# Kernel tuning notes

Hardware: AMD Instinct MI355X
Metric: run time of the kernel (lower is better)

Reference implementation:

```python
import jax, jax.numpy as jnp
import numpy as np

B, N, C = 4, 262144, 10
K_PRE, K_POST = 4096, 500          # before_nms_max, after_nms_max
ROI_THR, NMS_THR = 0.1, 0.01       # roi_threshold, nms_threshold


def setup_inputs() -> dict:
    key = jax.random.key(0)
    k1, k2, k3, k4 = jax.random.split(key, 4)
    # raw logits; sigmoid(-2 + noise) straddles roi_threshold=0.1 realistically
    cls = jax.random.normal(k1, (B, N, C), jnp.float32) - 2.0
    centers = jax.random.uniform(k2, (B, N, 3), jnp.float32, minval=-50.0, maxval=50.0)
    sizes = jax.random.uniform(k3, (B, N, 3), jnp.float32, minval=0.5, maxval=5.0)
    heading = jax.random.uniform(k4, (B, N, 1), jnp.float32, minval=-np.pi, maxval=np.pi)
    boxes = jnp.concatenate([centers, sizes, heading], axis=-1)  # (B, N, 7)
    return {"batch_cls_preds": cls, "batch_box_preds": boxes}


def _pairwise_bev_iou(b):
    # b: (K, 7) = [x, y, z, dx, dy, dz, heading]; BEV IoU (heading ignored,
    # axis-aligned approximation of the rotated-IoU CUDA kernel).
    x, y, dx, dy = b[:, 0], b[:, 1], b[:, 3], b[:, 4]
    x1, x2 = x - dx * 0.5, x + dx * 0.5
    y1, y2 = y - dy * 0.5, y + dy * 0.5
    ix = jnp.clip(jnp.minimum(x2[:, None], x2[None, :]) - jnp.maximum(x1[:, None], x1[None, :]), 0.0)
    iy = jnp.clip(jnp.minimum(y2[:, None], y2[None, :]) - jnp.maximum(y1[:, None], y1[None, :]), 0.0)
    inter = ix * iy                              # (K, K)
    area = dx * dy                               # (K,)
    union = area[:, None] + area[None, :] - inter
    return inter / jnp.maximum(union, 1e-6)


def _nms_one(scores, labels, boxes):
    # scores: (N,), labels: (N,) int32, boxes: (N, 7)
    s = jnp.where(scores > ROI_THR, scores, -1.0)       # score-threshold filter
    topv, topi = jax.lax.top_k(s, K_PRE)                # keep top before_nms_max
    tb = boxes[topi]                                     # (K_PRE, 7)
    tl = labels[topi]
    iou = _pairwise_bev_iou(tb)                          # (K_PRE, K_PRE)
    keep0 = topv > ROI_THR

    def body(i, keep):
        # a kept higher-score box i suppresses later boxes with IoU > thr
        sup = (iou[i] > NMS_THR) & (jnp.arange(K_PRE) > i) & keep[i]
        return keep & ~sup

    keep = jax.lax.fori_loop(0, K_PRE, body, keep0)
    kept_scores = jnp.where(keep, topv, -1.0)
    fv, fi = jax.lax.top_k(kept_scores, K_POST)          # after_nms_max slots
    m = fv > 0.0
    final_scores = jnp.where(m, fv, 0.0)                 # (K_POST,)
    final_boxes = tb[fi] * m[:, None].astype(tb.dtype)   # (K_POST, 7)
    final_labels = jnp.where(m, tl[fi], -1)              # (K_POST,)
    return final_scores, final_boxes, final_labels


def reference(batch_cls_preds, batch_box_preds):
    probs = jax.nn.sigmoid(batch_cls_preds)              # (B, N, C)
    scores = jnp.max(probs, axis=-1)                     # per-anchor best class score
    labels = jnp.argmax(probs, axis=-1).astype(jnp.int32)
    final_scores, final_boxes, final_labels = jax.vmap(_nms_one)(scores, labels, batch_box_preds)
    return final_scores, final_boxes, final_labels
```

## Files before the change

kernel.cpp:

```cpp
#include <hip/hip_runtime.h>
#include <stdint.h>

constexpr int B = 4;
constexpr int N = 262144;
constexpr int C = 10;
constexpr int KPRE = 4096;
constexpr int KPOST = 500;
constexpr float ROI_THR = 0.1f;
constexpr float NMS_THR = 0.01f;
constexpr int CAP = 8192;
constexpr int MASKW = KPRE / 64;
constexpr int RJT = 2;
constexpr int MAXP = 32;

__device__ __forceinline__ uint32_t f2k(float f) {
  uint32_t u = __float_as_uint(f);
  return (u & 0x80000000u) ? ~u : (u | 0x80000000u);
}
__device__ __forceinline__ float k2f(uint32_t k) {
  uint32_t u = (k & 0x80000000u) ? (k ^ 0x80000000u) : ~k;
  return __uint_as_float(u);
}
__device__ __forceinline__ float sigm(float x) { return 1.0f / (1.0f + expf(-x)); }

__device__ __forceinline__ void async_lds16(const void* g, void* l) {
  __builtin_amdgcn_global_load_lds((const __attribute__((address_space(1))) void*)g,
                                   (__attribute__((address_space(3))) void*)l, 16, 0, 0);
}

__device__ __forceinline__ uint2 select256(const uint32_t* __restrict__ h, uint32_t R,
                                           uint32_t* s, uint32_t* o2) {
  int t = threadIdx.x;
  s[t] = h[t];
  __syncthreads();
  for (int off = 1; off < 256; off <<= 1) {
    uint32_t v = s[t] + ((t + off < 256) ? s[t + off] : 0u);
    __syncthreads();
    s[t] = v;
    __syncthreads();
  }
  uint32_t suf = s[t];
  uint32_t sufn = (t < 255) ? s[t + 1] : 0u;
  if (suf >= R && R > sufn) {
    o2[0] = (uint32_t)t;
    o2[1] = R - sufn;
  }
  __syncthreads();
  uint2 r;
  r.x = o2[0];
  r.y = o2[1];
  __syncthreads();
  return r;
}

__global__ void scoreK(const float* __restrict__ cls, uint32_t* __restrict__ keys,
                       uint32_t* __restrict__ hist0) {
  __shared__ float ls[2560];
  __shared__ uint32_t h[256];
  int b = blockIdx.y;
  int t = threadIdx.x;
  h[t] = 0;
  size_t base = ((size_t)b * N + (size_t)blockIdx.x * 256) * C;
  const float2* g2 = (const float2*)(cls + base);
  float2* l2 = (float2*)ls;
#pragma unroll
  for (int r = 0; r < 5; ++r) l2[r * 256 + t] = g2[r * 256 + t];
  __syncthreads();
  const float* mine = ls + t * 10;
  float m = mine[0];
#pragma unroll
  for (int c = 1; c < C; ++c) m = fmaxf(m, mine[c]);
  float p = sigm(m);
  float sc = (p > ROI_THR) ? p : -1.0f;
  uint32_t k = f2k(sc);
  keys[(size_t)b * N + blockIdx.x * 256 + t] = k;
  atomicAdd(&h[k >> 24], 1u);
  __syncthreads();
  if (h[t]) atomicAdd(&hist0[b * 256 + t], h[t]);
}

__global__ void histP1K(const uint32_t* __restrict__ keys, const uint32_t* __restrict__ hist0,
                        uint32_t* __restrict__ hist1) {
  __shared__ uint32_t s[256];
  __shared__ uint32_t o2[2];
  __shared__ uint32_t h[256];
  int b = blockIdx.y;
  int t = threadIdx.x;
  uint2 s0 = select256(hist0 + b * 256, (uint32_t)KPRE, s, o2);
  h[t] = 0;
  __syncthreads();
  uint32_t pref = s0.x;
  const uint4* kb4 = (const uint4*)(keys + (size_t)b * N);
#pragma unroll
  for (int r = 0; r < 2; ++r) {
    uint4 kv = kb4[blockIdx.x * 512 + r * 256 + t];
#pragma unroll
    for (int j = 0; j < 4; ++j) {
      uint32_t k = (&kv.x)[j];
      if ((k >> 24) == pref) atomicAdd(&h[(k >> 16) & 255u], 1u);
    }
  }
  __syncthreads();
  if (h[t]) atomicAdd(&hist1[b * 256 + t], h[t]);
}

__global__ void compactK(const uint32_t* __restrict__ keys, const uint32_t* __restrict__ hist0,
                         const uint32_t* __restrict__ hist1, unsigned long long* __restrict__ list,
                         uint32_t* __restrict__ cnt) {
  __shared__ uint32_t s[256];
  __shared__ uint32_t o2[2];
  __shared__ uint32_t scan[256];
  __shared__ uint32_t baseSh;
  int b = blockIdx.y;
  int t = threadIdx.x;
  uint2 s0 = select256(hist0 + b * 256, (uint32_t)KPRE, s, o2);
  uint2 s1 = select256(hist1 + b * 256, s0.y, s, o2);
  uint32_t T = ((s0.x << 8) | s1.x) << 16;
  const uint4* kb4 = (const uint4*)(keys + (size_t)b * N);
  uint4 kv[4];
#pragma unroll
  for (int r = 0; r < 4; ++r) kv[r] = kb4[blockIdx.x * 1024 + r * 256 + t];
  uint32_t c = 0;
#pragma unroll
  for (int r = 0; r < 4; ++r)
#pragma unroll
    for (int j = 0; j < 4; ++j) c += ((&kv[r].x)[j] >= T) ? 1u : 0u;
  scan[t] = c;
  __syncthreads();
  for (int off = 1; off < 256; off <<= 1) {
    uint32_t v = scan[t] + ((t >= off) ? scan[t - off] : 0u);
    __syncthreads();
    scan[t] = v;
    __syncthreads();
  }
  uint32_t excl = scan[t] - c;
  if (t == 255) baseSh = atomicAdd(&cnt[b], scan[255]);
  __syncthreads();
  uint32_t pos = baseSh + excl;
#pragma unroll
  for (int r = 0; r < 4; ++r)
#pragma unroll
    for (int j = 0; j < 4; ++j) {
      uint32_t k = (&kv[r].x)[j];
      if (k >= T) {
        uint32_t n = (blockIdx.x * 1024 + r * 256 + t) * 4 + j;
        if (pos < CAP)
          list[(size_t)b * CAP + pos] = ((unsigned long long)k << 32) | (uint32_t)(~n);
        pos++;
      }
    }
}

__global__ void rankK(const unsigned long long* __restrict__ list, const uint32_t* __restrict__ cnt,
                      uint32_t* __restrict__ rank) {
  __shared__ unsigned long long lp[256];
  int b = blockIdx.z;
  int cc = (int)min(cnt[b], (uint32_t)CAP);
  if (blockIdx.x * 256 >= cc) return;
  int j0 = blockIdx.y * (256 * RJT);
  if (j0 >= cc) return;
  int i = blockIdx.x * 256 + threadIdx.x;
  unsigned long long pi = (i < cc) ? list[(size_t)b * CAP + i] : ~0ull;
  uint32_t c = 0;
#pragma unroll
  for (int tb = 0; tb < RJT; ++tb) {
    int j = j0 + tb * 256 + threadIdx.x;
    __syncthreads();
    lp[threadIdx.x] = (j < cc) ? list[(size_t)b * CAP + j] : 0ull;
    __syncthreads();
#pragma unroll 8
    for (int jj = 0; jj < 256; ++jj) c += (lp[jj] > pi) ? 1u : 0u;
  }
  if (i < cc && c) atomicAdd(&rank[(size_t)b * CAP + i], c);
}

__global__ void scatterK(const unsigned long long* __restrict__ list,
                         const uint32_t* __restrict__ cnt, const uint32_t* __restrict__ rank,
                         const float* __restrict__ boxes, float* __restrict__ sel_score,
                         uint32_t* __restrict__ sel_idx, float* __restrict__ sel_box) {
  int b = blockIdx.y;
  int p = blockIdx.x * 256 + threadIdx.x;
  uint32_t cc = min(cnt[b], (uint32_t)CAP);
  if (p >= (int)cc) return;
  unsigned long long pk = list[(size_t)b * CAP + p];
  uint32_t r = rank[(size_t)b * CAP + p];
  if (r >= (uint32_t)KPRE) return;
  uint32_t key = (uint32_t)(pk >> 32);
  uint32_t idx = ~(uint32_t)pk;
  sel_score[b * KPRE + r] = k2f(key);
  sel_idx[b * KPRE + r] = idx;
  const float* src = boxes + ((size_t)b * N + idx) * 7;
  float* dst = sel_box + ((size_t)b * KPRE + r) * 8;
#pragma unroll
  for (int c = 0; c < 7; ++c) dst[c] = src[c];
  dst[7] = 0.f;
}

__global__ void maskK(const float* __restrict__ sel_box, unsigned long long* __restrict__ mask,
                      unsigned long long* __restrict__ Tmat) {
  int b = blockIdx.z;
  int bi = blockIdx.x;
  int w = blockIdx.y;
  int t = threadIdx.x;
  int i = bi * 256 + t;
  int j0 = w * 64;
  unsigned long long* dst = mask + ((size_t)b * KPRE + i) * MASKW + w;
  if (j0 + 63 <= bi * 256) {
    *dst = 0ull;
    return;
  }
  __shared__ float4 jv[64];
  __shared__ float ja[64];
  if (t < 64) {
    const float4* bj = (const float4*)(sel_box + ((size_t)b * KPRE + j0 + t) * 8);
    float4 lo = bj[0], hi = bj[1];
    float xj = lo.x, yj = lo.y, dxj = lo.w, dyj = hi.x;
    float hxj = __fmul_rn(dxj, 0.5f), hyj = __fmul_rn(dyj, 0.5f);
    float4 v;
    v.x = __fsub_rn(xj, hxj);
    v.y = __fadd_rn(xj, hxj);
    v.z = __fsub_rn(yj, hyj);
    v.w = __fadd_rn(yj, hyj);
    jv[t] = v;
    ja[t] = __fmul_rn(dxj, dyj);
  }
  __syncthreads();
  const float4* myb = (const float4*)(sel_box + ((size_t)b * KPRE + i) * 8);
  float4 lo = myb[0], hi = myb[1];
  float x = lo.x, y = lo.y, dx = lo.w, dy = hi.x;
  float hx = __fmul_rn(dx, 0.5f), hy = __fmul_rn(dy, 0.5f);
  float x1i = __fsub_rn(x, hx), x2i = __fadd_rn(x, hx);
  float y1i = __fsub_rn(y, hy), y2i = __fadd_rn(y, hy);
  float ai = __fmul_rn(dx, dy);
  unsigned long long wacc = 0ull;
#pragma unroll 16
  for (int jj = 0; jj < 64; ++jj) {
    int j = j0 + jj;
    float4 v = jv[jj];
    float aj = ja[jj];
    float xx1 = fmaxf(x1i, v.x);
    float xx2 = fminf(x2i, v.y);
    float yy1 = fmaxf(y1i, v.z);
    float yy2 = fminf(y2i, v.w);
    float ix = fmaxf(__fsub_rn(xx2, xx1), 0.0f);
    float iy = fmaxf(__fsub_rn(yy2, yy1), 0.0f);
    float inter = __fmul_rn(ix, iy);
    float den = fmaxf(__fsub_rn(__fadd_rn(ai, aj), inter), 1e-6f);
    float q0 = __fmul_rn(NMS_THR, den);
    float d = __fsub_rn(inter, q0);
    bool sup = d > 0.0f;
    if (__builtin_expect(__any(fabsf(d) <= q0 * 1e-5f), 0)) {
      sup = (inter / den) > NMS_THR;
    }
    sup = sup && (j > i);
    wacc |= ((unsigned long long)(sup ? 1u : 0u)) << jj;
  }
  *dst = wacc;
  if ((w >> 2) == bi && (t >> 6) == (w & 3)) {
    int l = t & 63;
    unsigned long long m = wacc;
    unsigned long long T = 0ull;
#pragma unroll
    for (int j = 0; j < 64; ++j) {
      unsigned long long bj = __ballot(((m >> j) & 1ull) != 0ull);
      if (l == j) T = bj;
    }
    unsigned long long* trow = Tmat + ((size_t)b * 64 + w) * 128;
    trow[l] = T;
    trow[64 + l] = m;
  }
}

__global__ void nmsK(const unsigned long long* __restrict__ mask,
                     const unsigned long long* __restrict__ Tmat,
                     const float* __restrict__ sel_score,
                     uint32_t* __restrict__ kept_pos, uint32_t* __restrict__ kept_cnt) {
  __shared__ unsigned long long td[64][128];
  __shared__ uint32_t keptbuf[KPOST];
  int b = blockIdx.x;
  int t = threadIdx.x;

  const char* tsrc = (const char*)(Tmat + (size_t)b * 64 * 128);
  for (int g = 0; g < 64; ++g)
    async_lds16(tsrc + (size_t)g * 1024 + (size_t)t * 16, &td[g][0]);

  unsigned long long cand = 0ull;
  for (int k = 0; k < 64; ++k) {
    float s = sel_score[b * KPRE + k * 64 + t];
    unsigned long long bal = __ballot(s > ROI_THR);
    if (t == k) cand = bal;
  }
  asm volatile("s_waitcnt vmcnt(0)" ::: "memory");

  const unsigned long long* mb = mask + (size_t)b * KPRE * MASKW;
  unsigned long long remv = 0ull;
  unsigned long long r[MAXP];
#pragma unroll
  for (int a = 0; a < MAXP; ++a) r[a] = 0ull;
  int kc = 0;

  for (int g = 0; g < 64; ++g) {
#pragma unroll
    for (int a = 0; a < MAXP; ++a) remv |= r[a];

    unsigned long long cw = cand & ~remv;
    unsigned long long aw =
        ((unsigned long long)(uint32_t)__builtin_amdgcn_readlane((uint32_t)(cw >> 32), g) << 32) |
        (uint32_t)__builtin_amdgcn_readlane((uint32_t)cw, g);
    if (aw) {
      unsigned long long T = td[g][t];
      unsigned long long m = td[g][64 + t];
      unsigned long long K = __ballot((m & aw) != 0ull);
      unsigned long long alive = aw;
      unsigned long long rem = aw & K;
      if (rem) {
        bool deadf = ((aw >> t) & 1ull) == 0ull;
        while (rem) {
          int s = __ffsll((long long)rem) - 1;
          rem &= rem - 1ull;
          if ((alive >> s) & 1ull) {
            deadf = deadf || (((T >> s) & 1ull) != 0ull);
            alive = __ballot(!deadf);
            rem &= alive;
          }
        }
      }
      int grp = __popcll(alive);
      if ((alive >> t) & 1ull) {
        int rk = __popcll(alive & ((1ull << t) - 1ull));
        if (kc + rk < KPOST) keptbuf[kc + rk] = (uint32_t)(g * 64 + t);
      }
      kc += grp;
      unsigned long long a2 = alive;
      bool again = true;
      while (again) {
#pragma unroll
        for (int a = 0; a < MAXP; ++a) {
          if (a2) {
            int s2 = __ffsll((long long)a2) - 1;
            a2 &= a2 - 1ull;
            r[a] = mb[(size_t)(g * 64 + s2) * MASKW + t];
          } else {
            r[a] = 0ull;
          }
        }
        if (a2) {
#pragma unroll
          for (int a = 0; a < MAXP; ++a) {
            remv |= r[a];
            r[a] = 0ull;
          }
          again = true;
        } else {
          again = false;
        }
      }
      if (kc >= KPOST) break;
    } else {
#pragma unroll
      for (int a = 0; a < MAXP; ++a) r[a] = 0ull;
    }
  }
  asm volatile("s_waitcnt vmcnt(0)" ::: "memory");
  int kcc = min(kc, KPOST);
  for (int i = t; i < kcc; i += 64) kept_pos[b * KPOST + i] = keptbuf[i];
  if (t == 0) kept_cnt[b] = (uint32_t)kcc;
}

__global__ void outK(const float* __restrict__ cls,
                     const float* __restrict__ sel_score, const uint32_t* __restrict__ sel_idx,
                     const float* __restrict__ sel_box,
                     const uint32_t* __restrict__ kept_pos, const uint32_t* __restrict__ kept_cnt,
                     float* __restrict__ out) {
  int b = blockIdx.y;
  int s = blockIdx.x * blockDim.x + threadIdx.x;
  if (s >= KPOST) return;
  float* oS = out;
  float* oB = out + B * KPOST;
  float* oL = out + B * KPOST + B * KPOST * 7;
  uint32_t kcnt = kept_cnt[b];
  if (s < (int)kcnt) {
    uint32_t pos = kept_pos[b * KPOST + s];
    oS[b * KPOST + s] = sel_score[b * KPRE + pos];
    const float* box = sel_box + ((size_t)b * KPRE + pos) * 8;
    float* dst = oB + ((size_t)b * KPOST + s) * 7;
#pragma unroll
    for (int c = 0; c < 7; ++c) dst[c] = box[c];
    uint32_t idx = sel_idx[b * KPRE + pos];
    const float* p = cls + ((size_t)b * N + idx) * C;
    float bestv = sigm(p[0]);
    int bestc = 0;
#pragma unroll
    for (int c = 1; c < C; ++c) {
      float v = sigm(p[c]);
      if (v > bestv) { bestv = v; bestc = c; }
    }
    oL[b * KPOST + s] = (float)bestc;
  } else {
    oS[b * KPOST + s] = 0.0f;
    float* dst = oB + ((size_t)b * KPOST + s) * 7;
#pragma unroll
    for (int c = 0; c < 7; ++c) dst[c] = 0.0f;
    oL[b * KPOST + s] = -1.0f;
  }
}

__global__ void sentinelK(float* out, int n) {
  int i = blockIdx.x * blockDim.x + threadIdx.x;
  if (i < n) out[i] = 1337.0f;
}

extern "C" void kernel_launch(void* const* d_in, const int* in_sizes, int n_in,
                              void* d_out, int out_size, void* d_ws, size_t ws_size,
                              hipStream_t stream) {
  const float* cls = (const float*)d_in[0];
  const float* boxes = (const float*)d_in[1];
  float* out = (float*)d_out;

  char* ws = (char*)d_ws;
  size_t off = 0;
  auto alloc = [&](size_t bytes) -> void* {
    void* p = ws + off;
    off = (off + bytes + 255) & ~(size_t)255;
    return p;
  };
  unsigned long long* mask = (unsigned long long*)alloc((size_t)B * KPRE * MASKW * 8);
  unsigned long long* list = (unsigned long long*)alloc((size_t)B * CAP * 8);
  uint32_t* keys = (uint32_t*)alloc((size_t)B * N * 4);
  float* sel_box = (float*)alloc((size_t)B * KPRE * 8 * 4);
  float* sel_score = (float*)alloc((size_t)B * KPRE * 4);
  uint32_t* sel_idx = (uint32_t*)alloc((size_t)B * KPRE * 4);
  uint32_t* kept_pos = (uint32_t*)alloc((size_t)B * KPOST * 4);
  uint32_t* kept_cnt = (uint32_t*)alloc(B * 4);
  unsigned long long* Tmat = (unsigned long long*)alloc((size_t)B * 64 * 128 * 8);

  uint32_t* hist0 = (uint32_t*)mask;
  uint32_t* hist1 = hist0 + B * 256;
  uint32_t* cnt = hist1 + B * 256;
  uint32_t* rank = (uint32_t*)((char*)mask + 16384);
  size_t zbytes = 16384 + (size_t)B * CAP * 4;

  if (off > ws_size) {
    sentinelK<<<dim3((out_size + 255) / 256), 256, 0, stream>>>(out, out_size);
    return;
  }

  hipMemsetAsync(mask, 0, zbytes, stream);
  scoreK<<<dim3(N / 256, B), 256, 0, stream>>>(cls, keys, hist0);
  histP1K<<<dim3(N / 2048, B), 256, 0, stream>>>(keys, hist0, hist1);
  compactK<<<dim3(N / 4096, B), 256, 0, stream>>>(keys, hist0, hist1, list, cnt);
  rankK<<<dim3(CAP / 256, CAP / (256 * RJT), B), 256, 0, stream>>>(list, cnt, rank);
  scatterK<<<dim3(CAP / 256, B), 256, 0, stream>>>(list, cnt, rank, boxes, sel_score, sel_idx,
                                                   sel_box);
  maskK<<<dim3(16, 64, B), 256, 0, stream>>>(sel_box, mask, Tmat);
  nmsK<<<B, 64, 0, stream>>>(mask, Tmat, sel_score, kept_pos, kept_cnt);
  outK<<<dim3((KPOST + 255) / 256, B), 256, 0, stream>>>(cls, sel_score, sel_idx, sel_box,
                                                         kept_pos, kept_cnt, out);
}
```

Baseline: 142.5 us.

## Compute two mask rows per thread and zero mask via memset

The IoU mask kernel now handles two box rows per thread (512 rows per block), so each shared-memory column box is reused twice and half as many blocks launch. The per-iteration warp vote for near-threshold cases is replaced by an accumulated flag with one vote after the loop, plus a full exact-division fallback pass. A template specialisation drops the j>i check for tiles entirely above the diagonal. Lower-triangle tiles no longer write zeros; instead the whole mask buffer is memset up front, which adds a larger memset (about 8 MB) and extra register pressure.

```diff
diff --git a/kernel.cpp b/kernel.cpp
--- a/kernel.cpp
+++ b/kernel.cpp
@@ -196,21 +196,51 @@
   dst[7] = 0.f;
 }
 
+template <bool CHK>
+__device__ __forceinline__ void mask_inner(
+    int rel0, int rel1, const float4* __restrict__ jv, const float* __restrict__ ja,
+    float x1a, float x2a, float y1a, float y2a, float aa,
+    float x1b, float x2b, float y1b, float y2b, float ab,
+    uint32_t& lo0, uint32_t& hi0, uint32_t& lo1, uint32_t& hi1, uint32_t& band) {
+#pragma unroll 16
+  for (int jj = 0; jj < 64; ++jj) {
+    float4 v = jv[jj];
+    float aj = ja[jj];
+    float xx1 = fmaxf(x1a, v.x), xx2 = fminf(x2a, v.y);
+    float yy1 = fmaxf(y1a, v.z), yy2 = fminf(y2a, v.w);
+    float ix = fmaxf(__fsub_rn(xx2, xx1), 0.0f), iy = fmaxf(__fsub_rn(yy2, yy1), 0.0f);
+    float inter = __fmul_rn(ix, iy);
+    float den = fmaxf(__fsub_rn(__fadd_rn(aa, aj), inter), 1e-6f);
+    float q0 = __fmul_rn(NMS_THR, den);
+    band |= (fabsf(__fsub_rn(inter, q0)) <= __fmul_rn(q0, 1e-5f)) ? 1u : 0u;
+    bool sup = inter > q0;
+    if (CHK) sup = sup && (jj > rel0);
+    uint32_t bit = sup ? 1u : 0u;
+    if (jj < 32) lo0 |= bit << jj; else hi0 |= bit << (jj - 32);
+    float xx1b = fmaxf(x1b, v.x), xx2b = fminf(x2b, v.y);
+    float yy1b = fmaxf(y1b, v.z), yy2b = fminf(y2b, v.w);
+    float ixb = fmaxf(__fsub_rn(xx2b, xx1b), 0.0f), iyb = fmaxf(__fsub_rn(yy2b, yy1b), 0.0f);
+    float interb = __fmul_rn(ixb, iyb);
+    float denb = fmaxf(__fsub_rn(__fadd_rn(ab, aj), interb), 1e-6f);
+    float q0b = __fmul_rn(NMS_THR, denb);
+    band |= (fabsf(__fsub_rn(interb, q0b)) <= __fmul_rn(q0b, 1e-5f)) ? 1u : 0u;
+    bool supb = interb > q0b;
+    if (CHK) supb = supb && (jj > rel1);
+    uint32_t bitb = supb ? 1u : 0u;
+    if (jj < 32) lo1 |= bitb << jj; else hi1 |= bitb << (jj - 32);
+  }
+}
+
 __global__ void maskK(const float* __restrict__ sel_box, unsigned long long* __restrict__ mask,
                       unsigned long long* __restrict__ Tmat) {
   int b = blockIdx.z;
   int bi = blockIdx.x;
   int w = blockIdx.y;
   int t = threadIdx.x;
-  int i = bi * 256 + t;
-  int j0 = w * 64;
-  unsigned long long* dst = mask + ((size_t)b * KPRE + i) * MASKW + w;
-  if (j0 + 63 <= bi * 256) {
-    *dst = 0ull;
-    return;
-  }
+  if (w * 64 + 63 <= bi * 512) return;
   __shared__ float4 jv[64];
   __shared__ float ja[64];
+  int j0 = w * 64;
   if (t < 64) {
     const float4* bj = (const float4*)(sel_box + ((size_t)b * KPRE + j0 + t) * 8);
     float4 lo = bj[0], hi = bj[1];
@@ -225,40 +255,58 @@
     ja[t] = __fmul_rn(dxj, dyj);
   }
   __syncthreads();
-  const float4* myb = (const float4*)(sel_box + ((size_t)b * KPRE + i) * 8);
-  float4 lo = myb[0], hi = myb[1];
-  float x = lo.x, y = lo.y, dx = lo.w, dy = hi.x;
-  float hx = __fmul_rn(dx, 0.5f), hy = __fmul_rn(dy, 0.5f);
-  float x1i = __fsub_rn(x, hx), x2i = __fadd_rn(x, hx);
-  float y1i = __fsub_rn(y, hy), y2i = __fadd_rn(y, hy);
-  float ai = __fmul_rn(dx, dy);
-  unsigned long long wacc = 0ull;
-#pragma unroll 16
-  for (int jj = 0; jj < 64; ++jj) {
-    int j = j0 + jj;
-    float4 v = jv[jj];
-    float aj = ja[jj];
-    float xx1 = fmaxf(x1i, v.x);
-    float xx2 = fminf(x2i, v.y);
-    float yy1 = fmaxf(y1i, v.z);
-    float yy2 = fminf(y2i, v.w);
-    float ix = fmaxf(__fsub_rn(xx2, xx1), 0.0f);
-    float iy = fmaxf(__fsub_rn(yy2, yy1), 0.0f);
-    float inter = __fmul_rn(ix, iy);
-    float den = fmaxf(__fsub_rn(__fadd_rn(ai, aj), inter), 1e-6f);
-    float q0 = __fmul_rn(NMS_THR, den);
-    float d = __fsub_rn(inter, q0);
-    bool sup = d > 0.0f;
-    if (__builtin_expect(__any(fabsf(d) <= q0 * 1e-5f), 0)) {
-      sup = (inter / den) > NMS_THR;
+  int r0 = bi * 512 + t, r1 = r0 + 256;
+  const float4* ba = (const float4*)(sel_box + ((size_t)b * KPRE + r0) * 8);
+  const float4* bb = (const float4*)(sel_box + ((size_t)b * KPRE + r1) * 8);
+  float4 la = ba[0], ha = ba[1], lb = bb[0], hb = bb[1];
+  float hxa = __fmul_rn(la.w, 0.5f), hya = __fmul_rn(ha.x, 0.5f);
+  float x1a = __fsub_rn(la.x, hxa), x2a = __fadd_rn(la.x, hxa);
+  float y1a = __fsub_rn(la.y, hya), y2a = __fadd_rn(la.y, hya);
+  float aa = __fmul_rn(la.w, ha.x);
+  float hxb = __fmul_rn(lb.w, 0.5f), hyb = __fmul_rn(hb.x, 0.5f);
+  float x1b = __fsub_rn(lb.x, hxb), x2b = __fadd_rn(lb.x, hxb);
+  float y1b = __fsub_rn(lb.y, hyb), y2b = __fadd_rn(lb.y, hyb);
+  float ab = __fmul_rn(lb.w, hb.x);
+  int rel0 = r0 - j0, rel1 = r1 - j0;
+  uint32_t lo0 = 0, hi0 = 0, lo1 = 0, hi1 = 0, band = 0;
+  bool above = (j0 > bi * 512 + 511);
+  if (above)
+    mask_inner<false>(rel0, rel1, jv, ja, x1a, x2a, y1a, y2a, aa, x1b, x2b, y1b, y2b, ab,
+                      lo0, hi0, lo1, hi1, band);
+  else
+    mask_inner<true>(rel0, rel1, jv, ja, x1a, x2a, y1a, y2a, aa, x1b, x2b, y1b, y2b, ab,
+                     lo0, hi0, lo1, hi1, band);
+  if (__builtin_expect(__any(band != 0), 0)) {
+    lo0 = hi0 = lo1 = hi1 = 0;
+    for (int jj = 0; jj < 64; ++jj) {
+      float4 v = jv[jj];
+      float aj = ja[jj];
+      float xx1 = fmaxf(x1a, v.x), xx2 = fminf(x2a, v.y);
+      float yy1 = fmaxf(y1a, v.z), yy2 = fminf(y2a, v.w);
+      float ix = fmaxf(__fsub_rn(xx2, xx1), 0.0f), iy = fmaxf(__fsub_rn(yy2, yy1), 0.0f);
+      float inter = __fmul_rn(ix, iy);
+      float den = fmaxf(__fsub_rn(__fadd_rn(aa, aj), inter), 1e-6f);
+      bool sup = (inter / den) > NMS_THR && (jj > rel0);
+      uint32_t bit = sup ? 1u : 0u;
+      if (jj < 32) lo0 |= bit << jj; else hi0 |= bit << (jj - 32);
+      float xx1b = fmaxf(x1b, v.x), xx2b = fminf(x2b, v.y);
+      float yy1b = fmaxf(y1b, v.z), yy2b = fminf(y2b, v.w);
+      float ixb = fmaxf(__fsub_rn(xx2b, xx1b), 0.0f), iyb = fmaxf(__fsub_rn(yy2b, yy1b), 0.0f);
+      float interb = __fmul_rn(ixb, iyb);
+      float denb = fmaxf(__fsub_rn(__fadd_rn(ab, aj), interb), 1e-6f);
+      bool supb = (interb / denb) > NMS_THR && (jj > rel1);
+      uint32_t bitb = supb ? 1u : 0u;
+      if (jj < 32) lo1 |= bitb << jj; else hi1 |= bitb << (jj - 32);
     }
-    sup = sup && (j > i);
-    wacc |= ((unsigned long long)(sup ? 1u : 0u)) << jj;
-  }
-  *dst = wacc;
-  if ((w >> 2) == bi && (t >> 6) == (w & 3)) {
+  }
+  unsigned long long w0 = ((unsigned long long)hi0 << 32) | lo0;
+  unsigned long long w1 = ((unsigned long long)hi1 << 32) | lo1;
+  mask[((size_t)b * KPRE + r0) * MASKW + w] = w0;
+  mask[((size_t)b * KPRE + r1) * MASKW + w] = w1;
+  int d8 = w - 8 * bi;
+  if (d8 >= 0 && d8 < 8 && (t >> 6) == (d8 & 3)) {
     int l = t & 63;
-    unsigned long long m = wacc;
+    unsigned long long m = (d8 >> 2) ? w1 : w0;
     unsigned long long T = 0ull;
 #pragma unroll
     for (int j = 0; j < 64; ++j) {
@@ -424,7 +472,8 @@
     off = (off + bytes + 255) & ~(size_t)255;
     return p;
   };
-  unsigned long long* mask = (unsigned long long*)alloc((size_t)B * KPRE * MASKW * 8);
+  size_t mask_bytes = (size_t)B * KPRE * MASKW * 8;
+  unsigned long long* mask = (unsigned long long*)alloc(mask_bytes);
   unsigned long long* list = (unsigned long long*)alloc((size_t)B * CAP * 8);
   uint32_t* keys = (uint32_t*)alloc((size_t)B * N * 4);
   float* sel_box = (float*)alloc((size_t)B * KPRE * 8 * 4);
@@ -438,21 +487,20 @@
   uint32_t* hist1 = hist0 + B * 256;
   uint32_t* cnt = hist1 + B * 256;
   uint32_t* rank = (uint32_t*)((char*)mask + 16384);
-  size_t zbytes = 16384 + (size_t)B * CAP * 4;
 
   if (off > ws_size) {
     sentinelK<<<dim3((out_size + 255) / 256), 256, 0, stream>>>(out, out_size);
     return;
   }
 
-  hipMemsetAsync(mask, 0, zbytes, stream);
+  hipMemsetAsync(mask, 0, mask_bytes, stream);
   scoreK<<<dim3(N / 256, B), 256, 0, stream>>>(cls, keys, hist0);
   histP1K<<<dim3(N / 2048, B), 256, 0, stream>>>(keys, hist0, hist1);
   compactK<<<dim3(N / 4096, B), 256, 0, stream>>>(keys, hist0, hist1, list, cnt);
   rankK<<<dim3(CAP / 256, CAP / (256 * RJT), B), 256, 0, stream>>>(list, cnt, rank);
   scatterK<<<dim3(CAP / 256, B), 256, 0, stream>>>(list, cnt, rank, boxes, sel_score, sel_idx,
                                                    sel_box);
-  maskK<<<dim3(16, 64, B), 256, 0, stream>>>(sel_box, mask, Tmat);
+  maskK<<<dim3(8, 64, B), 256, 0, stream>>>(sel_box, mask, Tmat);
   nmsK<<<B, 64, 0, stream>>>(mask, Tmat, sel_score, kept_pos, kept_cnt);
   outK<<<dim3((KPOST + 255) / 256, B), 256, 0, stream>>>(cls, sel_score, sel_idx, sel_box,
                                                          kept_pos, kept_cnt, out);
```

Measured after the change: 144.2 us. Within noise of the previous version (+1.2%).
